# Optimization experiments

Measured on AMD Instinct MI355X. Metric: run time of the kernel, lower is better.

Reference implementation:

```python
import jax, jax.numpy as jnp
import numpy as np

B, T, V, NNZ = 4, 2048, 32000, 801
TAU, RARE, ALPHA = 0.8, 1.0, 0.7


def setup_inputs() -> dict:
    key = jax.random.key(0)
    k1, k2, k3, k4, k5 = jax.random.split(key, 5)
    logp = jax.nn.log_softmax(jax.random.normal(k1, (B, T, V), jnp.float32), axis=-1)
    target = jax.random.randint(k2, (B, T), 0, V, dtype=jnp.int32)
    mask = jnp.ones((B, T), jnp.float32)
    sim_values = jax.random.uniform(k3, (V, NNZ), jnp.float32)  # raw similarities in [0,1]
    idf_values = jax.random.uniform(k4, (V, NNZ), jnp.float32)
    sim_cols = jax.random.randint(k5, (V, NNZ), 0, V, dtype=jnp.int32)
    return {"logp": logp, "mask": mask, "sim_values": sim_values,
            "idf_values": idf_values, "target": target, "sim_cols": sim_cols}


def reference(logp, mask, sim_values, idf_values, target, sim_cols):
    N = B * T
    lp = logp.reshape(N, V)          # [N, V]
    rows = target.reshape(N)         # [N]
    m = mask.reshape(N)              # [N]

    # get_submatrix: per-target-row slice of the fixed-nnz sparse sim matrix
    vals = sim_values[rows] - 1.0 - TAU * RARE * idf_values[rows]  # [N, NNZ]
    # faithful to original: exp applied twice (exp(exp(v/tau)/tau))
    vals = jnp.exp(jnp.exp(vals / TAU) / TAU)
    sim = vals / jnp.sum(vals, axis=1, keepdims=True)              # row-normalized

    cols = sim_cols[rows]                                          # [N, NNZ]
    g = jnp.take_along_axis(lp, cols, axis=1)                      # gathered logp

    denom = jnp.sum(m)
    smooth_loss = -jnp.sum(g * sim) / denom                        # smoothed NLL
    ml_loss = -jnp.sum(jnp.take_along_axis(lp, rows[:, None], axis=1)[:, 0] * m) / denom
    return ALPHA * smooth_loss + (1.0 - ALPHA) * ml_loss
```

## Files before the change

### kernel.cpp

```cpp
#include <hip/hip_runtime.h>

#define VOCAB 32000
#define NNZ   801
#define NNZ_FULL 768
#define NNZ_TAIL 33
#define NROWS 8192
#define ROWS_PER_BLOCK 4

__device__ __forceinline__ float warp_reduce_add_f(float v) {
    #pragma unroll
    for (int off = 32; off > 0; off >>= 1) v += __shfl_down(v, off, 64);
    return v;
}

__global__ __launch_bounds__(256) void wordsmooth_main(
        const float* __restrict__ logp,
        const float* __restrict__ mask,
        const float* __restrict__ sim_values,
        const float* __restrict__ idf_values,
        const int*   __restrict__ target,
        const int*   __restrict__ sim_cols,
        double*      __restrict__ partials)
{
    const int lane = threadIdx.x & 63;
    const int wave = threadIdx.x >> 6;
    const int row  = blockIdx.x * ROWS_PER_BLOCK + wave;
    if (row >= NROWS) return;

    const int trow = target[row];
    const float* __restrict__ lp_row = logp + (size_t)row * VOCAB;
    const float* __restrict__ sv_p = sim_values + (size_t)trow * NNZ;
    const float* __restrict__ iv_p = idf_values + (size_t)trow * NNZ;
    const int*   __restrict__ sc_p = sim_cols   + (size_t)trow * NNZ;

    const float TAU_INV  = 1.25f;
    const float TAU_RARE = 0.8f;

    float s_v = 0.0f, s_gv = 0.0f;

    #pragma unroll 4
    for (int j = lane; j < NNZ_FULL; j += 64) {
        float sv = __builtin_nontemporal_load(sv_p + j);
        float iv = __builtin_nontemporal_load(iv_p + j);
        int   c  = __builtin_nontemporal_load(sc_p + j);
        float x   = (sv - 1.0f - TAU_RARE * iv) * TAU_INV;
        float val = __expf(__expf(x) * TAU_INV);
        float g   = lp_row[c];
        s_v  += val;
        s_gv += g * val;
    }
    if (lane < NNZ_TAIL) {
        int j = NNZ_FULL + lane;
        float sv = __builtin_nontemporal_load(sv_p + j);
        float iv = __builtin_nontemporal_load(iv_p + j);
        int   c  = __builtin_nontemporal_load(sc_p + j);
        float x   = (sv - 1.0f - TAU_RARE * iv) * TAU_INV;
        float val = __expf(__expf(x) * TAU_INV);
        float g   = lp_row[c];
        s_v  += val;
        s_gv += g * val;
    }

    s_v  = warp_reduce_add_f(s_v);
    s_gv = warp_reduce_add_f(s_gv);

    if (lane == 0) {
        float m = mask[row];
        partials[row]             = (double)(-s_gv / s_v);
        partials[NROWS + row]     = (double)(-lp_row[trow] * m);
        partials[2 * NROWS + row] = (double)m;
    }
}

__global__ __launch_bounds__(256) void wordsmooth_finalize(
        const double* __restrict__ partials, float* __restrict__ out)
{
    double s = 0.0, ml = 0.0, dn = 0.0;
    for (int i = threadIdx.x; i < NROWS; i += 256) {
        s  += partials[i];
        ml += partials[NROWS + i];
        dn += partials[2 * NROWS + i];
    }
    #pragma unroll
    for (int off = 32; off > 0; off >>= 1) {
        s  += __shfl_down(s,  off, 64);
        ml += __shfl_down(ml, off, 64);
        dn += __shfl_down(dn, off, 64);
    }
    __shared__ double sh[3][4];
    const int lane = threadIdx.x & 63;
    const int wave = threadIdx.x >> 6;
    if (lane == 0) { sh[0][wave] = s; sh[1][wave] = ml; sh[2][wave] = dn; }
    __syncthreads();
    if (threadIdx.x == 0) {
        double S = 0.0, M = 0.0, D = 0.0;
        #pragma unroll
        for (int w = 0; w < 4; ++w) { S += sh[0][w]; M += sh[1][w]; D += sh[2][w]; }
        const double ALPHA = 0.7;
        out[0] = (float)((ALPHA * S + (1.0 - ALPHA) * M) / D);
    }
}

extern "C" void kernel_launch(void* const* d_in, const int* in_sizes, int n_in,
                              void* d_out, int out_size, void* d_ws, size_t ws_size,
                              hipStream_t stream) {
    const float* logp       = (const float*)d_in[0];
    const float* mask       = (const float*)d_in[1];
    const float* sim_values = (const float*)d_in[2];
    const float* idf_values = (const float*)d_in[3];
    const int*   target     = (const int*)d_in[4];
    const int*   sim_cols   = (const int*)d_in[5];
    float* out = (float*)d_out;
    double* partials = (double*)d_ws;

    dim3 grid(NROWS / ROWS_PER_BLOCK);
    dim3 block(256);
    wordsmooth_main<<<grid, block, 0, stream>>>(logp, mask, sim_values, idf_values,
                                                target, sim_cols, partials);
    wordsmooth_finalize<<<1, 256, 0, stream>>>(partials, out);
}
```

Before: 1.355 ms.

## Stage logp half-rows in LDS and gather from shared memory

Each row is split across two blocks, and each block streams its 16000-float half of the logp row into LDS with coalesced float4 loads. The scattered column gathers then read from LDS, which turns random global accesses into full-row streaming. The per-half gathered sums are combined in the finalize kernel. This reads the whole logp tensor instead of only the touched entries, and it reads the sim, idf and column data twice per row.

Result: slower. 1.431 ms (+5.7%).

```diff
diff --git a/kernel.cpp b/kernel.cpp
--- a/kernel.cpp
+++ b/kernel.cpp
@@ -1,103 +1,101 @@
 #include <hip/hip_runtime.h>
 
 #define VOCAB 32000
+#define HALF  16000
 #define NNZ   801
-#define NNZ_FULL 768
-#define NNZ_TAIL 33
 #define NROWS 8192
-#define ROWS_PER_BLOCK 4
+#define TPB   512
 
-__device__ __forceinline__ float warp_reduce_add_f(float v) {
-    #pragma unroll
-    for (int off = 32; off > 0; off >>= 1) v += __shfl_down(v, off, 64);
-    return v;
-}
-
-__global__ __launch_bounds__(256) void wordsmooth_main(
+__global__ __launch_bounds__(TPB) void wordsmooth_main(
         const float* __restrict__ logp,
         const float* __restrict__ mask,
         const float* __restrict__ sim_values,
         const float* __restrict__ idf_values,
         const int*   __restrict__ target,
         const int*   __restrict__ sim_cols,
-        double*      __restrict__ partials)
+        float*       __restrict__ ws)
 {
-    const int lane = threadIdx.x & 63;
-    const int wave = threadIdx.x >> 6;
-    const int row  = blockIdx.x * ROWS_PER_BLOCK + wave;
-    if (row >= NROWS) return;
+    __shared__ __align__(16) float lds[HALF];
+    __shared__ float red[16];
+
+    const int row  = blockIdx.x >> 1;
+    const int half = blockIdx.x & 1;
+    const int tid  = threadIdx.x;
+    const int lo   = half * HALF;
+
+    const float4* __restrict__ src4 = (const float4*)(logp + (size_t)row * VOCAB + lo);
+    float4* dst4 = (float4*)lds;
+    #pragma unroll
+    for (int i = 0; i < 8; ++i) {
+        int idx = tid + i * TPB;
+        if (idx < HALF / 4) dst4[idx] = src4[idx];
+    }
+    __syncthreads();
 
     const int trow = target[row];
-    const float* __restrict__ lp_row = logp + (size_t)row * VOCAB;
-    const float* __restrict__ sv_p = sim_values + (size_t)trow * NNZ;
-    const float* __restrict__ iv_p = idf_values + (size_t)trow * NNZ;
-    const int*   __restrict__ sc_p = sim_cols   + (size_t)trow * NNZ;
-
-    const float TAU_INV  = 1.25f;
-    const float TAU_RARE = 0.8f;
+    const size_t base = (size_t)trow * NNZ;
+    const float* __restrict__ sv_p = sim_values + base;
+    const float* __restrict__ iv_p = idf_values + base;
+    const int*   __restrict__ sc_p = sim_cols   + base;
 
     float s_v = 0.0f, s_gv = 0.0f;
-
-    #pragma unroll 4
-    for (int j = lane; j < NNZ_FULL; j += 64) {
-        float sv = __builtin_nontemporal_load(sv_p + j);
-        float iv = __builtin_nontemporal_load(iv_p + j);
-        int   c  = __builtin_nontemporal_load(sc_p + j);
-        float x   = (sv - 1.0f - TAU_RARE * iv) * TAU_INV;
-        float val = __expf(__expf(x) * TAU_INV);
-        float g   = lp_row[c];
-        s_v  += val;
-        s_gv += g * val;
-    }
-    if (lane < NNZ_TAIL) {
-        int j = NNZ_FULL + lane;
-        float sv = __builtin_nontemporal_load(sv_p + j);
-        float iv = __builtin_nontemporal_load(iv_p + j);
-        int   c  = __builtin_nontemporal_load(sc_p + j);
-        float x   = (sv - 1.0f - TAU_RARE * iv) * TAU_INV;
-        float val = __expf(__expf(x) * TAU_INV);
-        float g   = lp_row[c];
-        s_v  += val;
-        s_gv += g * val;
+    for (int j = tid; j < NNZ; j += TPB) {
+        float sv = sv_p[j];
+        float iv = iv_p[j];
+        int   c  = sc_p[j];
+        float x   = __fmaf_rn(1.25f, sv, -1.25f) - iv;
+        float val = __expf(__expf(x) * 1.25f);
+        s_v += val;
+        int cl = c - lo;
+        if ((unsigned)cl < (unsigned)HALF) s_gv += lds[cl] * val;
     }
 
-    s_v  = warp_reduce_add_f(s_v);
-    s_gv = warp_reduce_add_f(s_gv);
-
-    if (lane == 0) {
-        float m = mask[row];
-        partials[row]             = (double)(-s_gv / s_v);
-        partials[NROWS + row]     = (double)(-lp_row[trow] * m);
-        partials[2 * NROWS + row] = (double)m;
+    #pragma unroll
+    for (int off = 32; off > 0; off >>= 1) {
+        s_v  += __shfl_down(s_v,  off, 64);
+        s_gv += __shfl_down(s_gv, off, 64);
+    }
+    const int wv = tid >> 6, ln = tid & 63;
+    if (ln == 0) { red[wv] = s_v; red[8 + wv] = s_gv; }
+    __syncthreads();
+    if (tid == 0) {
+        float tv = 0.0f, tg = 0.0f;
+        #pragma unroll
+        for (int w = 0; w < 8; ++w) { tv += red[w]; tg += red[8 + w]; }
+        ws[NROWS + half * NROWS + row] = tg;
+        if (half == 0) ws[row] = tv;
+        int cl = trow - lo;
+        if ((unsigned)cl < (unsigned)HALF) ws[3 * NROWS + row] = -lds[cl] * mask[row];
     }
 }
 
 __global__ __launch_bounds__(256) void wordsmooth_finalize(
-        const double* __restrict__ partials, float* __restrict__ out)
+        const float* __restrict__ ws, const float* __restrict__ mask,
+        float* __restrict__ out)
 {
-    double s = 0.0, ml = 0.0, dn = 0.0;
-    for (int i = threadIdx.x; i < NROWS; i += 256) {
-        s  += partials[i];
-        ml += partials[NROWS + i];
-        dn += partials[2 * NROWS + i];
+    double sm = 0.0, ml = 0.0, dn = 0.0;
+    for (int r = threadIdx.x; r < NROWS; r += 256) {
+        float svv = ws[r];
+        float gv  = ws[NROWS + r] + ws[2 * NROWS + r];
+        sm += (double)(-gv / svv);
+        ml += (double)ws[3 * NROWS + r];
+        dn += (double)mask[r];
     }
     #pragma unroll
     for (int off = 32; off > 0; off >>= 1) {
-        s  += __shfl_down(s,  off, 64);
+        sm += __shfl_down(sm, off, 64);
         ml += __shfl_down(ml, off, 64);
         dn += __shfl_down(dn, off, 64);
     }
     __shared__ double sh[3][4];
-    const int lane = threadIdx.x & 63;
-    const int wave = threadIdx.x >> 6;
-    if (lane == 0) { sh[0][wave] = s; sh[1][wave] = ml; sh[2][wave] = dn; }
+    const int ln = threadIdx.x & 63, wv = threadIdx.x >> 6;
+    if (ln == 0) { sh[0][wv] = sm; sh[1][wv] = ml; sh[2][wv] = dn; }
     __syncthreads();
     if (threadIdx.x == 0) {
         double S = 0.0, M = 0.0, D = 0.0;
         #pragma unroll
         for (int w = 0; w < 4; ++w) { S += sh[0][w]; M += sh[1][w]; D += sh[2][w]; }
-        const double ALPHA = 0.7;
-        out[0] = (float)((ALPHA * S + (1.0 - ALPHA) * M) / D);
+        out[0] = (float)((0.7 * S + 0.3 * M) / D);
     }
 }
 
@@ -111,11 +109,9 @@
     const int*   target     = (const int*)d_in[4];
     const int*   sim_cols   = (const int*)d_in[5];
     float* out = (float*)d_out;
-    double* partials = (double*)d_ws;
+    float* ws  = (float*)d_ws;
 
-    dim3 grid(NROWS / ROWS_PER_BLOCK);
-    dim3 block(256);
-    wordsmooth_main<<<grid, block, 0, stream>>>(logp, mask, sim_values, idf_values,
-                                                target, sim_cols, partials);
-    wordsmooth_finalize<<<1, 256, 0, stream>>>(partials, out);
+    wordsmooth_main<<<dim3(NROWS * 2), dim3(TPB), 0, stream>>>(
+        logp, mask, sim_values, idf_values, target, sim_cols, ws);
+    wordsmooth_finalize<<<dim3(1), dim3(256), 0, stream>>>(ws, mask, out);
 }
```
